# Kernel optimization log

Measured on AMD Instinct MI355X. Metric: run time of the kernel, lower is better.

Reference implementation:

```python
import jax, jax.numpy as jnp
import numpy as np
import math

B, C, N = 8, 512, 4096

def _phi(x):
    return jax.nn.relu(x) + 1.0

def _layernorm(x, g, b, eps=1e-6):
    mu = jnp.mean(x, axis=-1, keepdims=True)
    var = jnp.var(x, axis=-1, keepdims=True)
    return (x - mu) * jax.lax.rsqrt(var + eps) * g + b

def setup_inputs() -> dict:
    key = jax.random.key(0)
    ks = jax.random.split(key, 8)
    s = 1.0 / math.sqrt(C)
    x = jax.random.normal(ks[0], (B, C, N), dtype=jnp.float32)
    w_qk = jax.random.normal(ks[1], (C, C), dtype=jnp.float32) * s   # shared q/k conv1d(k=1) weight
    w_v = jax.random.normal(ks[2], (C, C), dtype=jnp.float32) * s
    w_phi = jax.random.normal(ks[3], (C, C), dtype=jnp.float32) * s  # phi_proj Linear weight [out,in]
    g1 = jnp.ones((C,), jnp.float32); b1 = jnp.zeros((C,), jnp.float32)
    w1 = jax.random.normal(ks[4], (4 * C, C), dtype=jnp.float32) * s
    bb1 = jnp.zeros((4 * C,), jnp.float32)
    w2 = jax.random.normal(ks[5], (C, 4 * C), dtype=jnp.float32) * (1.0 / math.sqrt(4 * C))
    bb2 = jnp.zeros((C,), jnp.float32)
    g2 = jnp.ones((C,), jnp.float32); b2 = jnp.zeros((C,), jnp.float32)
    return {"x": x, "w_qk": w_qk, "w_v": w_v, "w_phi": w_phi,
            "g1": g1, "b1": b1, "w1": w1, "bb1": bb1, "w2": w2, "bb2": bb2,
            "g2": g2, "b2": b2}

def reference(x, w_qk, w_v, w_phi, g1, b1, w1, bb1, w2, bb2, g2, b2):
    # x: [B,C,N]
    res = x
    q = _phi(jnp.einsum('oc,bcn->bon', w_qk, x))      # shared weight for q and k
    k = _phi(jnp.einsum('oc,bcn->bon', w_qk, x))
    v = jnp.einsum('oc,bcn->bon', w_v, x)
    phi_x = jnp.einsum('oc,bcn->bon', w_phi, x)       # phi_proj applied over channel dim
    # alpha gating
    Qg = jnp.mean(q, axis=2, keepdims=True)           # [B,C,1]
    n_pts = q.shape[-1]
    alpha = jax.nn.softmax(jnp.sum(Qg * k, axis=1, keepdims=True), axis=-1) * n_pts  # [B,1,N]
    k_hat = k * alpha
    # linear attention
    c = q.shape[1]
    kv = jnp.einsum('bcn,bdn->bcd', k_hat, v) / math.sqrt(c)   # [B,C,C]
    k_sum = jnp.sum(k_hat, axis=-1)                            # [B,C]
    z = 1.0 / (jnp.einsum('bcn,bc->bn', q, k_sum)[:, None, :] + 1e-6)  # [B,1,N]
    y = jnp.einsum('bcn,bcd->bdn', q, kv) * z                  # [B,C,N]
    y = y * phi_x
    h = _layernorm(jnp.transpose(res + y, (0, 2, 1)), g1, b1)  # [B,N,C]
    # FFN
    h = h + jnp.einsum('bnf,cf->bnc', jax.nn.relu(jnp.einsum('bnc,fc->bnf', h, w1) + bb1), w2) + bb2
    h = jax.nn.relu(_layernorm(h, g2, b2))
    return jnp.transpose(h, (0, 2, 1))  # [B,C,N]
```

## Files before the change

### kernel.cpp

```cpp
#include <hip/hip_runtime.h>
#include <stdint.h>


#define DEVI static __device__ __forceinline__

typedef short bf16x8 __attribute__((ext_vector_type(8)));
typedef float f32x4  __attribute__((ext_vector_type(4)));

DEVI float b2f(uint16_t u){ union { uint32_t i; float f; } v; v.i = ((uint32_t)u) << 16; return v.f; }
DEVI uint16_t f2b(float f){
  union { float f; uint32_t i; } v; v.f = f;
  uint32_t i = v.i;
  return (uint16_t)((i + 0x7FFFu + ((i >> 16) & 1u)) >> 16);
}

struct GP {
  const uint16_t* A;  long sAb;
  const uint16_t* Bm; long sBb;
  int K;
  int nOffB;
  int nOffO;
  int klen, nsplit;
  uint16_t* outH; uint16_t* outH2; uint16_t* outH3; long sOHb;
  float*    outF; long sOFb;
  const float* x;
  const uint16_t* f; long sFb;
  const float* bias;
  const float* tt; const float* mu; const float* rstd; const float* g1; const float* b1;
  float* accOut;
};

template<int EPI>
__global__ __launch_bounds__(256, 2) void gemm_nt(GP p){
  __shared__ __align__(16) char smem[34816];
  uint16_t* lA = (uint16_t*)smem;
  uint16_t* lB = (uint16_t*)(smem + 16384);

  const int t  = threadIdx.x;
  const int wv = t >> 6, ln = t & 63;
  const int bz = blockIdx.z;
  const int batch = bz / p.nsplit, sk = bz - batch * p.nsplit;
  const int m0 = blockIdx.y * 128, n0 = blockIdx.x * 128;
  const uint16_t* Ab = p.A  + (size_t)batch * p.sAb;
  const uint16_t* Bt = p.Bm + (size_t)batch * p.sBb;
  const int kbeg = sk * p.klen, kend = kbeg + p.klen;

  f32x4 acc[4][4];
  #pragma unroll
  for(int i = 0; i < 4; i++)
    #pragma unroll
    for(int j = 0; j < 4; j++) acc[i][j] = (f32x4){0.f, 0.f, 0.f, 0.f};

  const int rA = t >> 3;
  const int cA = (t & 7) * 8;
  const int lm = ln & 15, kg = ln >> 4;
  const int wr = (wv >> 1) * 64, wc = (wv & 1) * 64;

  for(int kt = kbeg; kt < kend; kt += 64){
    const uint16_t* ga = Ab + (size_t)(m0 + rA) * p.K + kt + cA;
    const uint16_t* gb = Bt + (size_t)(n0 + p.nOffB + rA) * p.K + kt + cA;
    #pragma unroll
    for(int i = 0; i < 4; i++){
      __builtin_amdgcn_global_load_lds(
        (const __attribute__((address_space(1))) uint32_t*)(ga + (size_t)i * 32 * p.K),
        (__attribute__((address_space(3))) uint32_t*)(smem + wv * 1024 + i * 4096), 16, 0, 0);
    }
    #pragma unroll
    for(int i = 0; i < 4; i++){
      __builtin_amdgcn_global_load_lds(
        (const __attribute__((address_space(1))) uint32_t*)(gb + (size_t)i * 32 * p.K),
        (__attribute__((address_space(3))) uint32_t*)(smem + 16384 + wv * 1024 + i * 4096), 16, 0, 0);
    }
    __syncthreads();
    #pragma unroll
    for(int ks = 0; ks < 64; ks += 32){
      bf16x8 af[4], bfr[4];
      #pragma unroll
      for(int i = 0; i < 4; i++){
        af[i]  = *(const bf16x8*)&lA[(wr + i * 16 + lm) * 64 + ks + kg * 8];
        bfr[i] = *(const bf16x8*)&lB[(wc + i * 16 + lm) * 64 + ks + kg * 8];
      }
      #pragma unroll
      for(int mi = 0; mi < 4; mi++)
        #pragma unroll
        for(int ni = 0; ni < 4; ni++)
          acc[mi][ni] = __builtin_amdgcn_mfma_f32_16x16x32_bf16(af[mi], bfr[ni], acc[mi][ni], 0, 0, 0);
    }
    __syncthreads();
  }

  const int rb2 = (ln >> 4) * 4;
  const int gmb = m0 + wr + rb2;
  const int gnb = n0 + wc + lm;

  if constexpr (EPI == 0){
    const int which = m0 >> 9;
    uint16_t* Ob = (which == 0 ? p.outH : which == 1 ? p.outH2 : p.outH3)
                 + (size_t)batch * ((size_t)512 * 4096);
    float* O32 = p.outF + (size_t)batch * p.sOFb;
    const bool isp = (which == 0);
    #pragma unroll
    for(int mi = 0; mi < 4; mi++)
      #pragma unroll
      for(int i = 0; i < 4; i++){
        int row = (gmb + mi * 16 + i) & 511;
        #pragma unroll
        for(int ni = 0; ni < 4; ni++){
          float v = acc[mi][ni][i];
          if(isp){
            v = fmaxf(v, 0.f) + 1.f;
            O32[(size_t)row * 4096 + gnb + ni * 16] = v;
          }
          Ob[(size_t)row * 4096 + gnb + ni * 16] = f2b(v);
        }
      }
  } else if constexpr (EPI == 1){
    float* O = p.accOut + ((size_t)sk * 8 + batch) * (512 * 512);
    #pragma unroll
    for(int mi = 0; mi < 4; mi++)
      #pragma unroll
      for(int i = 0; i < 4; i++){
        size_t row = (size_t)(gmb + mi * 16 + i) * 512;
        #pragma unroll
        for(int ni = 0; ni < 4; ni++)
          O[row + gnb + ni * 16] = acc[mi][ni][i];
      }
  } else if constexpr (EPI == 2){
    float* O = p.outF + (size_t)batch * p.sOFb;
    const float* X = p.x + (size_t)batch * ((size_t)512 * 4096);
    const uint16_t* Fp = p.f + (size_t)batch * p.sFb;
    #pragma unroll
    for(int mi = 0; mi < 4; mi++)
      #pragma unroll
      for(int i = 0; i < 4; i++){
        size_t row = (size_t)(gmb + mi * 16 + i) * 4096;
        #pragma unroll
        for(int ni = 0; ni < 4; ni++){
          size_t o = row + gnb + ni * 16;
          O[o] = X[o] + acc[mi][ni][i] * b2f(Fp[o]);
        }
      }
  } else if constexpr (EPI == 4 || EPI == 5){
    float*    OF = p.outF + (size_t)batch * p.sOFb;
    uint16_t* OH = p.outH + (size_t)batch * p.sOHb;
    const float* T = p.tt + (size_t)batch * ((size_t)512 * 4096);
    #pragma unroll
    for(int mi = 0; mi < 4; mi++)
      #pragma unroll
      for(int i = 0; i < 4; i++){
        int gm = gmb + mi * 16 + i;
        float g = p.g1[gm], bb = p.b1[gm], bs = p.bias[gm];
        #pragma unroll
        for(int ni = 0; ni < 4; ni++){
          int gn = gnb + ni * 16 + p.nOffO;
          size_t o  = (size_t)gm * 4096 + gn;
          size_t bn = (size_t)batch * 4096 + gn;
          float h = (T[o] - p.mu[bn]) * p.rstd[bn] * g + bb;
          float val = acc[mi][ni][i] + bs + h;
          if constexpr (EPI == 4) OF[o] = val;
          else                    OH[o] = f2b(val);
        }
      }
  } else {
    uint16_t* lT = (uint16_t*)smem;
    #pragma unroll
    for(int mi = 0; mi < 4; mi++){
      int fl = wr + mi * 16 + rb2;
      #pragma unroll
      for(int ni = 0; ni < 4; ni++){
        int nl = wc + ni * 16 + lm;
        ushort4 pk;
        pk.x = f2b(fmaxf(acc[mi][ni][0] + p.bias[m0 + fl + 0], 0.f));
        pk.y = f2b(fmaxf(acc[mi][ni][1] + p.bias[m0 + fl + 1], 0.f));
        pk.z = f2b(fmaxf(acc[mi][ni][2] + p.bias[m0 + fl + 2], 0.f));
        pk.w = f2b(fmaxf(acc[mi][ni][3] + p.bias[m0 + fl + 3], 0.f));
        *(ushort4*)&lT[nl * 136 + fl] = pk;
      }
    }
    __syncthreads();
    uint16_t* O = p.outH + (size_t)batch * p.sOHb;
    #pragma unroll
    for(int ps = 0; ps < 8; ps++){
      int nl  = ps * 16 + (t >> 4);
      int flc = (t & 15) * 8;
      uint4 v = *(const uint4*)&lT[nl * 136 + flc];
      *(uint4*)&O[(size_t)(n0 + nl) * 2048 + m0 + flc] = v;
    }
  }
}


__global__ void k_wprep(const float* wqk, const float* wv, const float* wphi,
                        const float* w1, const float* w2,
                        uint16_t* Wcat, uint16_t* w1b, uint16_t* w2b){
  int idx = blockIdx.x * 256 + threadIdx.x;
  const int nA = 1536 * 512, nB = 2048 * 512, nC = 512 * 2048;
  if(idx < nA){
    int which = idx / (512 * 512), r = idx % (512 * 512);
    const float* s = which == 0 ? wqk : (which == 1 ? wv : wphi);
    Wcat[idx] = f2b(s[r]);
  } else if(idx < nA + nB){
    int r = idx - nA; w1b[r] = f2b(w1[r]);
  } else if(idx < nA + nB + nC){
    int r = idx - nA - nB; w2b[r] = f2b(w2[r]);
  }
}

template<int OP, typename ST>
__global__ void k_transpose(const ST* src, uint16_t* dst, int RS, int CS,
                            long sSrcB, long sDstB,
                            const float* v1, const float* v2, const float* v3, const float* v4){
  __shared__ float tile[64 * 65];
  int b = blockIdx.z;
  int rb = blockIdx.y * 64, cb = blockIdx.x * 64;
  const ST* S = src + (size_t)b * sSrcB;
  uint16_t* D = dst + (size_t)b * sDstB;
  int t = threadIdx.x;
  int tr = t >> 4, tc4 = (t & 15) * 4;
  #pragma unroll
  for(int ps = 0; ps < 4; ps++){
    int r = ps * 16 + tr;
    size_t sa = (size_t)(rb + r) * CS + cb + tc4;
    float x0, x1, x2, x3;
    if constexpr (sizeof(ST) == 4){
      float4 vv = *(const float4*)&S[sa];
      x0 = vv.x; x1 = vv.y; x2 = vv.z; x3 = vv.w;
    } else {
      ushort4 vv = *(const ushort4*)&S[sa];
      x0 = b2f(vv.x); x1 = b2f(vv.y); x2 = b2f(vv.z); x3 = b2f(vv.w);
    }
    tile[r * 65 + tc4 + 0] = x0; tile[r * 65 + tc4 + 1] = x1;
    tile[r * 65 + tc4 + 2] = x2; tile[r * 65 + tc4 + 3] = x3;
  }
  __syncthreads();
  #pragma unroll
  for(int ps = 0; ps < 4; ps++){
    int ccl = ps * 16 + tr;
    int dr = cb + ccl;
    float m = 0.f, rs = 0.f;
    if constexpr (OP == 1){ m = v1[(size_t)b * CS + dr]; }
    if constexpr (OP == 2){ m = v1[(size_t)b * CS + dr]; rs = v2[(size_t)b * CS + dr]; }
    ushort4 o;
    float vals[4];
    #pragma unroll
    for(int j = 0; j < 4; j++){
      float v = tile[(tc4 + j) * 65 + ccl];
      if constexpr (OP == 1) v *= m;
      if constexpr (OP == 2) v = (v - m) * rs * v3[rb + tc4 + j] + v4[rb + tc4 + j];
      vals[j] = v;
    }
    o.x = f2b(vals[0]); o.y = f2b(vals[1]); o.z = f2b(vals[2]); o.w = f2b(vals[3]);
    *(ushort4*)&D[(size_t)dr * RS + rb + tc4] = o;
  }
}

__global__ void k_rowred(const uint16_t* src, long sB, float* out, float scale){
  int gw = blockIdx.x * 4 + (threadIdx.x >> 6);
  int ln = threadIdx.x & 63;
  int b = gw >> 9, r = gw & 511;
  const uint16_t* S = src + (size_t)b * sB + (size_t)r * 4096;
  float acc = 0.f;
  #pragma unroll
  for(int i = 0; i < 8; i++){
    const uint16_t* q = S + i * 512 + ln * 8;
    ushort4 a = *(const ushort4*)q;
    ushort4 c = *(const ushort4*)(q + 4);
    acc += b2f(a.x) + b2f(a.y) + b2f(a.z) + b2f(a.w)
         + b2f(c.x) + b2f(c.y) + b2f(c.z) + b2f(c.w);
  }
  #pragma unroll
  for(int off = 32; off; off >>= 1) acc += __shfl_down(acc, off, 64);
  if(ln == 0) out[gw] = acc * scale;
}

template<int OP, typename ST>
__global__ void k_coldot(const ST* mat, long sB, const float* vec, float* out){
  __shared__ float red[256];
  int b = blockIdx.y;
  int n = blockIdx.x * 64 + (threadIdx.x & 63);
  int cc = threadIdx.x >> 6;
  const ST* M = mat + (size_t)b * sB + (size_t)cc * 128 * 4096 + n;
  const float* V = vec + b * 512 + cc * 128;
  float acc = 0.f;
  #pragma unroll 4
  for(int ci = 0; ci < 128; ci++){
    float v;
    if constexpr (sizeof(ST) == 4) v = (float)M[(size_t)ci * 4096];
    else                           v = b2f((uint16_t)M[(size_t)ci * 4096]);
    acc += v * V[ci];
  }
  red[threadIdx.x] = acc;
  __syncthreads();
  if(threadIdx.x < 64){
    float s = red[threadIdx.x] + red[threadIdx.x + 64] + red[threadIdx.x + 128] + red[threadIdx.x + 192];
    if constexpr (OP == 0) out[(size_t)b * 4096 + n] = s;
    else                   out[(size_t)b * 4096 + n] = 1.f / (s + 1e-6f);
  }
}

__global__ void k_softmax(const float* s, float* alpha){
  __shared__ float red[16];
  int b = blockIdx.x, t = threadIdx.x;
  const float* S = s + (size_t)b * 4096;
  float4 v = *(const float4*)&S[t * 4];
  float mx = fmaxf(fmaxf(v.x, v.y), fmaxf(v.z, v.w));
  #pragma unroll
  for(int off = 32; off; off >>= 1) mx = fmaxf(mx, __shfl_down(mx, off, 64));
  if((t & 63) == 0) red[t >> 6] = mx;
  __syncthreads();
  float bm = red[0];
  #pragma unroll
  for(int i = 1; i < 16; i++) bm = fmaxf(bm, red[i]);
  float e0 = __expf(v.x - bm), e1 = __expf(v.y - bm), e2 = __expf(v.z - bm), e3 = __expf(v.w - bm);
  float sm = e0 + e1 + e2 + e3;
  #pragma unroll
  for(int off = 32; off; off >>= 1) sm += __shfl_down(sm, off, 64);
  __syncthreads();
  if((t & 63) == 0) red[t >> 6] = sm;
  __syncthreads();
  float tot = red[0];
  #pragma unroll
  for(int i = 1; i < 16; i++) tot += red[i];
  float sc = 4096.f / tot;
  float4 o; o.x = e0 * sc; o.y = e1 * sc; o.z = e2 * sc; o.w = e3 * sc;
  *(float4*)&alpha[(size_t)b * 4096 + t * 4] = o;
}

__global__ void k_phat(const uint16_t* pb, const float* alpha, uint16_t* phat){
  size_t idx = ((size_t)blockIdx.x * 256 + threadIdx.x) * 4;
  const size_t per = (size_t)512 * 4096;
  int b = (int)(idx / per); int n = (int)(idx & 4095);
  ushort4 pv = *(const ushort4*)&pb[idx];
  float4 av = *(const float4*)&alpha[(size_t)b * 4096 + n];
  ushort4 o;
  o.x = f2b(b2f(pv.x) * av.x); o.y = f2b(b2f(pv.y) * av.y);
  o.z = f2b(b2f(pv.z) * av.z); o.w = f2b(b2f(pv.w) * av.w);
  *(ushort4*)&phat[idx] = o;
}

template<typename ST>
__global__ void k_lnstats(const ST* src, float* mu, float* rstd){
  __shared__ float redS[256], redQ[256];
  int b = blockIdx.y;
  int n = blockIdx.x * 64 + (threadIdx.x & 63);
  int cc = threadIdx.x >> 6;
  const ST* S = src + (size_t)b * 512 * 4096 + (size_t)cc * 128 * 4096 + n;
  float s = 0.f, q = 0.f;
  #pragma unroll 4
  for(int ci = 0; ci < 128; ci++){
    float v;
    if constexpr (sizeof(ST) == 4) v = (float)S[(size_t)ci * 4096];
    else                           v = b2f((uint16_t)S[(size_t)ci * 4096]);
    s += v; q += v * v;
  }
  redS[threadIdx.x] = s; redQ[threadIdx.x] = q;
  __syncthreads();
  if(threadIdx.x < 64){
    s = redS[threadIdx.x] + redS[threadIdx.x + 64] + redS[threadIdx.x + 128] + redS[threadIdx.x + 192];
    q = redQ[threadIdx.x] + redQ[threadIdx.x + 64] + redQ[threadIdx.x + 128] + redQ[threadIdx.x + 192];
    float m = s * (1.f / 512.f);
    float var = q * (1.f / 512.f) - m * m;
    mu[(size_t)b * 4096 + n] = m;
    rstd[(size_t)b * 4096 + n] = rsqrtf(var + 1e-6f);
  }
}

__global__ void k_kvfin(const float* acc4, uint16_t* kvT){
  __shared__ float tile[64 * 65];
  int b = blockIdx.z; int cb = blockIdx.y * 64, db = blockIdx.x * 64;
  int t = threadIdx.x; int tr = t >> 4, tc4 = (t & 15) * 4;
  const size_t per = (size_t)8 * 512 * 512;
  const float* S = acc4 + (size_t)b * 512 * 512;
  #pragma unroll
  for(int ps = 0; ps < 4; ps++){
    int r = ps * 16 + tr;
    size_t a = (size_t)(cb + r) * 512 + db + tc4;
    float4 v0 = *(const float4*)&S[a];
    float4 v1 = *(const float4*)&S[per + a];
    float4 v2 = *(const float4*)&S[2 * per + a];
    float4 v3 = *(const float4*)&S[3 * per + a];
    tile[r * 65 + tc4 + 0] = v0.x + v1.x + v2.x + v3.x;
    tile[r * 65 + tc4 + 1] = v0.y + v1.y + v2.y + v3.y;
    tile[r * 65 + tc4 + 2] = v0.z + v1.z + v2.z + v3.z;
    tile[r * 65 + tc4 + 3] = v0.w + v1.w + v2.w + v3.w;
  }
  __syncthreads();
  const float sc = 0.044194173824159216f;
  #pragma unroll
  for(int ps = 0; ps < 4; ps++){
    int dl = ps * 16 + tr;
    ushort4 o;
    o.x = f2b(tile[(tc4 + 0) * 65 + dl] * sc);
    o.y = f2b(tile[(tc4 + 1) * 65 + dl] * sc);
    o.z = f2b(tile[(tc4 + 2) * 65 + dl] * sc);
    o.w = f2b(tile[(tc4 + 3) * 65 + dl] * sc);
    *(ushort4*)&kvT[(size_t)b * 512 * 512 + (size_t)(db + dl) * 512 + cb + tc4] = o;
  }
}

template<typename ST>
__global__ void k_final(const ST* t2, const float* mu2, const float* rstd2,
                        const float* g2, const float* b2v, float* out){
  size_t idx = ((size_t)blockIdx.x * 256 + threadIdx.x) * 4;
  const size_t per = (size_t)512 * 4096;
  int b = (int)(idx / per); size_t rem = idx % per;
  int c = (int)(rem >> 12);
  float4 v;
  if constexpr (sizeof(ST) == 4){
    v = *(const float4*)&t2[idx];
  } else {
    ushort4 u = *(const ushort4*)&t2[idx];
    v.x = b2f(u.x); v.y = b2f(u.y); v.z = b2f(u.z); v.w = b2f(u.w);
  }
  size_t bn = (size_t)b * 4096 + (rem & 4095);
  float4 m = *(const float4*)&mu2[bn];
  float4 r = *(const float4*)&rstd2[bn];
  float g = g2[c], bb = b2v[c];
  float4 o;
  o.x = fmaxf((v.x - m.x) * r.x * g + bb, 0.f);
  o.y = fmaxf((v.y - m.y) * r.y * g + bb, 0.f);
  o.z = fmaxf((v.z - m.z) * r.z * g + bb, 0.f);
  o.w = fmaxf((v.w - m.w) * r.w * g + bb, 0.f);
  *(float4*)&out[idx] = o;
}

extern "C" void kernel_launch(void* const* d_in, const int* in_sizes, int n_in,
                              void* d_out, int out_size, void* d_ws, size_t ws_size,
                              hipStream_t stream){
  const float* x    = (const float*)d_in[0];
  const float* wqk  = (const float*)d_in[1];
  const float* wv   = (const float*)d_in[2];
  const float* wphi = (const float*)d_in[3];
  const float* g1   = (const float*)d_in[4];
  const float* b1   = (const float*)d_in[5];
  const float* w1   = (const float*)d_in[6];
  const float* bb1  = (const float*)d_in[7];
  const float* w2   = (const float*)d_in[8];
  const float* bb2  = (const float*)d_in[9];
  const float* g2   = (const float*)d_in[10];
  const float* b2   = (const float*)d_in[11];
  float* out = (float*)d_out;

  char* w = (char*)d_ws;
  const size_t MB32 = (size_t)33554432;
  const size_t WTOT = ((size_t)1536 * 512 * 2 + 255 & ~(size_t)255)
                    + ((size_t)2048 * 512 * 2) + ((size_t)512 * 2048 * 2)
                    + 2 * ((8 * 512 * 4 + 255) & ~(size_t)255)
                    + 8 * ((8 * 4096 * 4 + 255) & ~(size_t)255) + 4096;
  const size_t needFull = 7 * MB32 + WTOT;
  const size_t needCmp  = 6 * MB32 + 4 * 1048576 + WTOT;

  int mode;
  if(ws_size >= needFull) mode = 0;
  else if(ws_size >= needCmp) mode = 1;
  else mode = 2;
  if(mode == 2){
    hipMemsetAsync(d_out, 0, (size_t)out_size * sizeof(float), stream);
    return;
  }

  uint16_t* xT    = (uint16_t*)(w + 0);
  uint16_t* fb    = (uint16_t*)(w + MB32);
  uint16_t* vb    = (uint16_t*)(w + 2 * MB32);
  uint16_t* pb    = (uint16_t*)(w + 3 * MB32);
  uint16_t* phat  = (uint16_t*)(w + 4 * MB32);
  float*    kvac4 = (float*)   (w + 5 * MB32);
  uint16_t* kvT   = (uint16_t*)(w + 6 * MB32);
  float*    p32  = (float*)(w + 4 * MB32);
  float*    tb   = (float*)(w + 2 * MB32);
  uint16_t* uTh  = (uint16_t*)(w + 0);
  uint16_t* hT   = phat;
  float*    t2f  = (float*)(w + 5 * MB32);
  uint16_t* t2b  = (uint16_t*)(w + 5 * MB32);
  uint16_t* pTz  = xT;
  size_t off = (mode == 0) ? 7 * MB32 : 6 * MB32 + 4 * 1048576;
  auto alloc = [&](size_t bytes) -> void* {
    void* pp = w + off; off += (bytes + 255) & ~(size_t)255; return pp;
  };
  uint16_t* Wcat = (uint16_t*)alloc((size_t)1536 * 512 * 2);
  uint16_t* w1b  = (uint16_t*)alloc((size_t)2048 * 512 * 2);
  uint16_t* w2b  = (uint16_t*)alloc((size_t)512 * 2048 * 2);
  float* Qg    = (float*)alloc(8 * 512 * 4);
  float* ksum  = (float*)alloc(8 * 512 * 4);
  float* sbuf  = (float*)alloc(8 * 4096 * 4);
  float* alpha = (float*)alloc(8 * 4096 * 4);
  float* zbuf  = (float*)alloc(8 * 4096 * 4);
  float* mu    = (float*)alloc(8 * 4096 * 4);
  float* rstd  = (float*)alloc(8 * 4096 * 4);
  float* mu2   = (float*)alloc(8 * 4096 * 4);
  float* rstd2 = (float*)alloc(8 * 4096 * 4);
  const long sCN = (long)512 * 4096;

  k_wprep<<<11264, 256, 0, stream>>>(wqk, wv, wphi, w1, w2, Wcat, w1b, w2b);
  k_transpose<0, float><<<dim3(64, 8, 8), 256, 0, stream>>>(
      x, xT, 512, 4096, sCN, sCN, nullptr, nullptr, nullptr, nullptr);

  GP gp1{}; gp1.A = Wcat; gp1.sAb = 0; gp1.Bm = xT; gp1.sBb = sCN;
  gp1.K = 512; gp1.klen = 512; gp1.nsplit = 1;
  gp1.outH = pb; gp1.outH2 = vb; gp1.outH3 = fb;
  gp1.outF = p32; gp1.sOFb = sCN;
  gemm_nt<0><<<dim3(32, 12, 8), 256, 0, stream>>>(gp1);

  k_rowred<<<1024, 256, 0, stream>>>(pb, sCN, Qg, 1.f / 4096.f);
  k_coldot<0, float><<<dim3(64, 8), 256, 0, stream>>>(p32, sCN, Qg, sbuf);
  k_softmax<<<8, 1024, 0, stream>>>(sbuf, alpha);
  k_phat<<<16384, 256, 0, stream>>>(pb, alpha, phat);
  k_rowred<<<1024, 256, 0, stream>>>(phat, sCN, ksum, 1.f);
  k_coldot<1, uint16_t><<<dim3(64, 8), 256, 0, stream>>>(pb, sCN, ksum, zbuf);
  k_transpose<1, uint16_t><<<dim3(64, 8, 8), 256, 0, stream>>>(
      pb, pTz, 512, 4096, sCN, sCN, zbuf, nullptr, nullptr, nullptr);

  GP gp2{}; gp2.A = phat; gp2.sAb = sCN; gp2.Bm = vb; gp2.sBb = sCN;
  gp2.K = 4096; gp2.klen = 1024; gp2.nsplit = 4; gp2.accOut = kvac4;
  gemm_nt<1><<<dim3(4, 4, 32), 256, 0, stream>>>(gp2);
  k_kvfin<<<dim3(8, 8, 8), 256, 0, stream>>>(kvac4, kvT);

  GP gp3{}; gp3.A = kvT; gp3.sAb = (long)512 * 512; gp3.Bm = pTz; gp3.sBb = sCN;
  gp3.K = 512; gp3.klen = 512; gp3.nsplit = 1;
  gp3.outF = tb; gp3.sOFb = sCN; gp3.x = x;
  gp3.f = fb; gp3.sFb = sCN;
  gemm_nt<2><<<dim3(32, 4, 8), 256, 0, stream>>>(gp3);

  k_lnstats<float><<<dim3(64, 8), 256, 0, stream>>>(tb, mu, rstd);
  k_transpose<2, float><<<dim3(64, 8, 8), 256, 0, stream>>>(
      tb, hT, 512, 4096, sCN, sCN, mu, rstd, g1, b1);

  for(int h = 0; h < 2; h++){
    GP gp4{}; gp4.A = w1b; gp4.sAb = 0; gp4.Bm = hT; gp4.sBb = sCN;
    gp4.K = 512; gp4.klen = 512; gp4.nsplit = 1; gp4.nOffB = h * 2048;
    gp4.outH = uTh; gp4.sOHb = (long)2048 * 2048; gp4.bias = bb1;
    gemm_nt<3><<<dim3(16, 16, 8), 256, 0, stream>>>(gp4);

    GP gp5{}; gp5.A = w2b; gp5.sAb = 0; gp5.Bm = uTh; gp5.sBb = (long)2048 * 2048;
    gp5.K = 2048; gp5.klen = 2048; gp5.nsplit = 1; gp5.nOffO = h * 2048;
    gp5.bias = bb2;
    gp5.tt = tb; gp5.mu = mu; gp5.rstd = rstd; gp5.g1 = g1; gp5.b1 = b1;
    if(mode == 0){
      gp5.outF = t2f; gp5.sOFb = sCN;
      gemm_nt<4><<<dim3(16, 4, 8), 256, 0, stream>>>(gp5);
    } else {
      gp5.outH = t2b; gp5.sOHb = sCN;
      gemm_nt<5><<<dim3(16, 4, 8), 256, 0, stream>>>(gp5);
    }
  }

  if(mode == 0){
    k_lnstats<float><<<dim3(64, 8), 256, 0, stream>>>(t2f, mu2, rstd2);
    k_final<float><<<16384, 256, 0, stream>>>(t2f, mu2, rstd2, g2, b2, out);
  } else {
    k_lnstats<uint16_t><<<dim3(64, 8), 256, 0, stream>>>(t2b, mu2, rstd2);
    k_final<uint16_t><<<16384, 256, 0, stream>>>(t2b, mu2, rstd2, g2, b2, out);
  }
}
```

Baseline: 700.5 us.

## Precompute normalized residual in transpose and run FFN as single full-N pass

The layernorm-1 transpose now also writes a bf16 copy of the normalized activations in [C,N] layout. The FFN second GEMM epilogue adds this copy directly instead of re-reading the fp32 pre-norm tensor plus mu/rstd/g1/b1 per element. The FFN is also no longer split into two N-halves: one larger launch of each GEMM covers all N, with a full-size intermediate buffer in place of the old chunked one. This removes the workspace mode switch, always storing the FFN output in bf16, which may cost some precision compared with the fp32 path used when workspace allowed.

```diff
diff --git a/kernel.cpp b/kernel.cpp
--- a/kernel.cpp
+++ b/kernel.cpp
@@ -18,15 +18,12 @@
   const uint16_t* A;  long sAb;
   const uint16_t* Bm; long sBb;
   int K;
-  int nOffB;
-  int nOffO;
   int klen, nsplit;
   uint16_t* outH; uint16_t* outH2; uint16_t* outH3; long sOHb;
   float*    outF; long sOFb;
   const float* x;
   const uint16_t* f; long sFb;
   const float* bias;
-  const float* tt; const float* mu; const float* rstd; const float* g1; const float* b1;
   float* accOut;
 };
 
@@ -58,7 +55,7 @@
 
   for(int kt = kbeg; kt < kend; kt += 64){
     const uint16_t* ga = Ab + (size_t)(m0 + rA) * p.K + kt + cA;
-    const uint16_t* gb = Bt + (size_t)(n0 + p.nOffB + rA) * p.K + kt + cA;
+    const uint16_t* gb = Bt + (size_t)(n0 + rA) * p.K + kt + cA;
     #pragma unroll
     for(int i = 0; i < 4; i++){
       __builtin_amdgcn_global_load_lds(
@@ -140,25 +137,19 @@
           O[o] = X[o] + acc[mi][ni][i] * b2f(Fp[o]);
         }
       }
-  } else if constexpr (EPI == 4 || EPI == 5){
-    float*    OF = p.outF + (size_t)batch * p.sOFb;
+  } else if constexpr (EPI == 6){
     uint16_t* OH = p.outH + (size_t)batch * p.sOHb;
-    const float* T = p.tt + (size_t)batch * ((size_t)512 * 4096);
+    const uint16_t* H = p.f + (size_t)batch * p.sFb;
     #pragma unroll
     for(int mi = 0; mi < 4; mi++)
       #pragma unroll
       for(int i = 0; i < 4; i++){
         int gm = gmb + mi * 16 + i;
-        float g = p.g1[gm], bb = p.b1[gm], bs = p.bias[gm];
+        float bs = p.bias[gm];
         #pragma unroll
         for(int ni = 0; ni < 4; ni++){
-          int gn = gnb + ni * 16 + p.nOffO;
-          size_t o  = (size_t)gm * 4096 + gn;
-          size_t bn = (size_t)batch * 4096 + gn;
-          float h = (T[o] - p.mu[bn]) * p.rstd[bn] * g + bb;
-          float val = acc[mi][ni][i] + bs + h;
-          if constexpr (EPI == 4) OF[o] = val;
-          else                    OH[o] = f2b(val);
+          size_t o = (size_t)gm * 4096 + gnb + ni * 16;
+          OH[o] = f2b(acc[mi][ni][i] + bs + b2f(H[o]));
         }
       }
   } else {
@@ -207,8 +198,8 @@
 }
 
 template<int OP, typename ST>
-__global__ void k_transpose(const ST* src, uint16_t* dst, int RS, int CS,
-                            long sSrcB, long sDstB,
+__global__ void k_transpose(const ST* src, uint16_t* dst, uint16_t* dst2,
+                            int RS, int CS, long sSrcB, long sDstB,
                             const float* v1, const float* v2, const float* v3, const float* v4){
   __shared__ float tile[64 * 65];
   int b = blockIdx.z;
@@ -229,6 +220,17 @@
       ushort4 vv = *(const ushort4*)&S[sa];
       x0 = b2f(vv.x); x1 = b2f(vv.y); x2 = b2f(vv.z); x3 = b2f(vv.w);
     }
+    if constexpr (OP == 2){
+      float4 m4 = *(const float4*)&v1[(size_t)b * CS + cb + tc4];
+      float4 r4 = *(const float4*)&v2[(size_t)b * CS + cb + tc4];
+      float gg = v3[rb + r], bv = v4[rb + r];
+      x0 = (x0 - m4.x) * r4.x * gg + bv;
+      x1 = (x1 - m4.y) * r4.y * gg + bv;
+      x2 = (x2 - m4.z) * r4.z * gg + bv;
+      x3 = (x3 - m4.w) * r4.w * gg + bv;
+      ushort4 hh; hh.x = f2b(x0); hh.y = f2b(x1); hh.z = f2b(x2); hh.w = f2b(x3);
+      *(ushort4*)&dst2[(size_t)b * ((size_t)RS * CS) + (size_t)(rb + r) * CS + cb + tc4] = hh;
+    }
     tile[r * 65 + tc4 + 0] = x0; tile[r * 65 + tc4 + 1] = x1;
     tile[r * 65 + tc4 + 2] = x2; tile[r * 65 + tc4 + 3] = x3;
   }
@@ -237,16 +239,14 @@
   for(int ps = 0; ps < 4; ps++){
     int ccl = ps * 16 + tr;
     int dr = cb + ccl;
-    float m = 0.f, rs = 0.f;
+    float m = 0.f;
     if constexpr (OP == 1){ m = v1[(size_t)b * CS + dr]; }
-    if constexpr (OP == 2){ m = v1[(size_t)b * CS + dr]; rs = v2[(size_t)b * CS + dr]; }
     ushort4 o;
     float vals[4];
     #pragma unroll
     for(int j = 0; j < 4; j++){
       float v = tile[(tc4 + j) * 65 + ccl];
       if constexpr (OP == 1) v *= m;
-      if constexpr (OP == 2) v = (v - m) * rs * v3[rb + tc4 + j] + v4[rb + tc4 + j];
       vals[j] = v;
     }
     o.x = f2b(vals[0]); o.y = f2b(vals[1]); o.z = f2b(vals[2]); o.w = f2b(vals[3]);
@@ -447,14 +447,8 @@
                     + ((size_t)2048 * 512 * 2) + ((size_t)512 * 2048 * 2)
                     + 2 * ((8 * 512 * 4 + 255) & ~(size_t)255)
                     + 8 * ((8 * 4096 * 4 + 255) & ~(size_t)255) + 4096;
-  const size_t needFull = 7 * MB32 + WTOT;
-  const size_t needCmp  = 6 * MB32 + 4 * 1048576 + WTOT;
-
-  int mode;
-  if(ws_size >= needFull) mode = 0;
-  else if(ws_size >= needCmp) mode = 1;
-  else mode = 2;
-  if(mode == 2){
+  const size_t need = 6 * MB32 + 4 * 1048576 + WTOT;
+  if(ws_size < need){
     hipMemsetAsync(d_out, 0, (size_t)out_size * sizeof(float), stream);
     return;
   }
@@ -466,14 +460,14 @@
   uint16_t* phat  = (uint16_t*)(w + 4 * MB32);
   float*    kvac4 = (float*)   (w + 5 * MB32);
   uint16_t* kvT   = (uint16_t*)(w + 6 * MB32);
-  float*    p32  = (float*)(w + 4 * MB32);
-  float*    tb   = (float*)(w + 2 * MB32);
-  uint16_t* uTh  = (uint16_t*)(w + 0);
-  uint16_t* hT   = phat;
-  float*    t2f  = (float*)(w + 5 * MB32);
-  uint16_t* t2b  = (uint16_t*)(w + 5 * MB32);
-  uint16_t* pTz  = xT;
-  size_t off = (mode == 0) ? 7 * MB32 : 6 * MB32 + 4 * 1048576;
+  float*    p32 = (float*)(w + 4 * MB32);
+  float*    tb  = (float*)(w + 2 * MB32);
+  uint16_t* hT  = phat;
+  uint16_t* t2b = phat;
+  uint16_t* hb  = (uint16_t*)(w + 5 * MB32);
+  uint16_t* uT  = (uint16_t*)(w + 0);
+  uint16_t* pTz = xT;
+  size_t off = 6 * MB32 + 4 * 1048576;
   auto alloc = [&](size_t bytes) -> void* {
     void* pp = w + off; off += (bytes + 255) & ~(size_t)255; return pp;
   };
@@ -493,7 +487,7 @@
 
   k_wprep<<<11264, 256, 0, stream>>>(wqk, wv, wphi, w1, w2, Wcat, w1b, w2b);
   k_transpose<0, float><<<dim3(64, 8, 8), 256, 0, stream>>>(
-      x, xT, 512, 4096, sCN, sCN, nullptr, nullptr, nullptr, nullptr);
+      x, xT, nullptr, 512, 4096, sCN, sCN, nullptr, nullptr, nullptr, nullptr);
 
   GP gp1{}; gp1.A = Wcat; gp1.sAb = 0; gp1.Bm = xT; gp1.sBb = sCN;
   gp1.K = 512; gp1.klen = 512; gp1.nsplit = 1;
@@ -508,7 +502,7 @@
   k_rowred<<<1024, 256, 0, stream>>>(phat, sCN, ksum, 1.f);
   k_coldot<1, uint16_t><<<dim3(64, 8), 256, 0, stream>>>(pb, sCN, ksum, zbuf);
   k_transpose<1, uint16_t><<<dim3(64, 8, 8), 256, 0, stream>>>(
-      pb, pTz, 512, 4096, sCN, sCN, zbuf, nullptr, nullptr, nullptr);
+      pb, pTz, nullptr, 512, 4096, sCN, sCN, zbuf, nullptr, nullptr, nullptr);
 
   GP gp2{}; gp2.A = phat; gp2.sAb = sCN; gp2.Bm = vb; gp2.sBb = sCN;
   gp2.K = 4096; gp2.klen = 1024; gp2.nsplit = 4; gp2.accOut = kvac4;
@@ -523,32 +517,19 @@
 
   k_lnstats<float><<<dim3(64, 8), 256, 0, stream>>>(tb, mu, rstd);
   k_transpose<2, float><<<dim3(64, 8, 8), 256, 0, stream>>>(
-      tb, hT, 512, 4096, sCN, sCN, mu, rstd, g1, b1);
-
-  for(int h = 0; h < 2; h++){
-    GP gp4{}; gp4.A = w1b; gp4.sAb = 0; gp4.Bm = hT; gp4.sBb = sCN;
-    gp4.K = 512; gp4.klen = 512; gp4.nsplit = 1; gp4.nOffB = h * 2048;
-    gp4.outH = uTh; gp4.sOHb = (long)2048 * 2048; gp4.bias = bb1;
-    gemm_nt<3><<<dim3(16, 16, 8), 256, 0, stream>>>(gp4);
-
-    GP gp5{}; gp5.A = w2b; gp5.sAb = 0; gp5.Bm = uTh; gp5.sBb = (long)2048 * 2048;
-    gp5.K = 2048; gp5.klen = 2048; gp5.nsplit = 1; gp5.nOffO = h * 2048;
-    gp5.bias = bb2;
-    gp5.tt = tb; gp5.mu = mu; gp5.rstd = rstd; gp5.g1 = g1; gp5.b1 = b1;
-    if(mode == 0){
-      gp5.outF = t2f; gp5.sOFb = sCN;
-      gemm_nt<4><<<dim3(16, 4, 8), 256, 0, stream>>>(gp5);
-    } else {
-      gp5.outH = t2b; gp5.sOHb = sCN;
-      gemm_nt<5><<<dim3(16, 4, 8), 256, 0, stream>>>(gp5);
-    }
-  }
-
-  if(mode == 0){
-    k_lnstats<float><<<dim3(64, 8), 256, 0, stream>>>(t2f, mu2, rstd2);
-    k_final<float><<<16384, 256, 0, stream>>>(t2f, mu2, rstd2, g2, b2, out);
-  } else {
-    k_lnstats<uint16_t><<<dim3(64, 8), 256, 0, stream>>>(t2b, mu2, rstd2);
-    k_final<uint16_t><<<16384, 256, 0, stream>>>(t2b, mu2, rstd2, g2, b2, out);
-  }
-}
+      tb, hT, hb, 512, 4096, sCN, sCN, mu, rstd, g1, b1);
+
+  GP gp4{}; gp4.A = w1b; gp4.sAb = 0; gp4.Bm = hT; gp4.sBb = sCN;
+  gp4.K = 512; gp4.klen = 512; gp4.nsplit = 1;
+  gp4.outH = uT; gp4.sOHb = (long)4096 * 2048; gp4.bias = bb1;
+  gemm_nt<3><<<dim3(32, 16, 8), 256, 0, stream>>>(gp4);
+
+  GP gp5{}; gp5.A = w2b; gp5.sAb = 0; gp5.Bm = uT; gp5.sBb = (long)4096 * 2048;
+  gp5.K = 2048; gp5.klen = 2048; gp5.nsplit = 1;
+  gp5.outH = t2b; gp5.sOHb = sCN; gp5.bias = bb2;
+  gp5.f = hb; gp5.sFb = sCN;
+  gemm_nt<6><<<dim3(32, 4, 8), 256, 0, stream>>>(gp5);
+
+  k_lnstats<uint16_t><<<dim3(64, 8), 256, 0, stream>>>(t2b, mu2, rstd2);
+  k_final<uint16_t><<<16384, 256, 0, stream>>>(t2b, mu2, rstd2, g2, b2, out);
+}
```

New measurement: 620.8 us. -11.4%, faster.
